# Kernel tuning notes

Hardware: AMD Instinct MI355X
Metric: run time of the kernel (lower is better)

Reference implementation:

```python
import jax, jax.numpy as jnp
import numpy as np

D_K = 64
SCALE = 1.0 / np.sqrt(D_K).astype(np.float32)


def setup_inputs() -> dict:
    key = jax.random.key(0)
    kq, kk, kv = jax.random.split(key, 3)
    B, S, D = 4, 2048, 512
    q = jax.random.normal(kq, (B, S, D), dtype=jnp.float32)
    k = jax.random.normal(kk, (B, S, D), dtype=jnp.float32)
    v = jax.random.normal(kv, (B, S, D), dtype=jnp.float32)
    return {"q": q, "k": k, "v": v}


def reference(q, k, v):
    # n_head == 1: the per-head strided slices are the full tensors.
    # Original computes BOTH 'new_k' (scaled q@k^T) and 'new_v' (unscaled q@k^T);
    # note: v is never used in the original forward math (faithful reproduction).
    qk = jnp.einsum('bsd,btd->bst', q, k)           # [B, S, S]
    scores = qk * SCALE                              # new_k
    attn = jax.nn.softmax(scores, axis=2)            # softmax over dim 2
    # dropout with p=0.1 is identity in eval / deterministic reference
    out = jnp.matmul(attn, qk)                       # attn @ new_v -> [B, S, S]
    return out
```

## Files before the change

kernel.cpp:

```cpp
#include <hip/hip_runtime.h>
#include <hip/hip_bf16.h>
#include <stdint.h>


#define SS 2048
#define DD 512
#define BATCH 4
#define NTB 8
#define NT2A 32

typedef __attribute__((ext_vector_type(8))) short short8;
typedef __attribute__((ext_vector_type(8))) _Float16 half8;
typedef __attribute__((ext_vector_type(4))) float floatx4;
typedef __attribute__((ext_vector_type(4))) float float4v;
typedef __attribute__((ext_vector_type(4))) unsigned int uintx4;

#define GLOBAL_AS const __attribute__((address_space(1)))
#define LDS_AS __attribute__((address_space(3)))

__device__ __forceinline__ uint32_t pk2h(float x, float y) {
    _Float16 hx = (_Float16)x, hy = (_Float16)y;
    union { _Float16 h; uint16_t u; } cx, cy;
    cx.h = hx; cy.h = hy;
    return (uint32_t)cx.u | ((uint32_t)cy.u << 16);
}
__device__ __forceinline__ float h2f(uint32_t ubits) {
    union { uint16_t u; _Float16 h; } c; c.u = (uint16_t)ubits; return (float)c.h;
}
__device__ __forceinline__ uint16_t f2h(float f) {
    union { _Float16 h; uint16_t u; } c; c.h = (_Float16)f; return c.u;
}

union PackU { uint32_t u[4]; short8 s8; };

__global__ __launch_bounds__(256) void prep_kernel(
    const float* __restrict__ Q, const float* __restrict__ K,
    uint16_t* __restrict__ qT, uint16_t* __restrict__ qH,
    uint16_t* __restrict__ kH)
{
    const int b   = blockIdx.z;
    const int tid = threadIdx.x;

    if (blockIdx.y >= 8) {
        const float* src = (blockIdx.y == 8) ? (K + (size_t)b * SS * DD)
                                             : (Q + (size_t)b * SS * DD);
        uint16_t* dst = (blockIdx.y == 8) ? (kH + (size_t)b * SS * DD)
                                          : (qH + (size_t)b * SS * DD);
        const int g0 = blockIdx.x * 256 + tid;
#pragma unroll
        for (int i = 0; i < 16; ++i) {
            const int g = g0 + i * 8192;
            const float4v* s4 = (const float4v*)(src + (size_t)g * 8);
            float4v x0 = s4[0], x1 = s4[1];
            PackU p;
            p.u[0] = pk2h(x0[0], x0[1]);
            p.u[1] = pk2h(x0[2], x0[3]);
            p.u[2] = pk2h(x1[0], x1[1]);
            p.u[3] = pk2h(x1[2], x1[3]);
            *(short8*)(dst + (size_t)g * 8) = p.s8;
        }
        return;
    }

    const int u0 = blockIdx.x * 64;
    const int d0 = blockIdx.y * 64;
    const float* qb = Q + (size_t)b * SS * DD;
    uint16_t* qTb = qT + (size_t)b * DD * SS;

    __shared__ uint16_t T[64 * 66];

    {
        const int r  = tid >> 2;
        const int c4 = (tid & 3) * 16;
        const float* src = qb + (size_t)(u0 + r) * DD + d0 + c4;
        float4v x0 = *(const float4v*)(src + 0);
        float4v x1 = *(const float4v*)(src + 4);
        float4v x2 = *(const float4v*)(src + 8);
        float4v x3 = *(const float4v*)(src + 12);
        uint32_t* tw = (uint32_t*)&T[r * 66 + c4];
        tw[0] = pk2h(x0[0], x0[1]); tw[1] = pk2h(x0[2], x0[3]);
        tw[2] = pk2h(x1[0], x1[1]); tw[3] = pk2h(x1[2], x1[3]);
        tw[4] = pk2h(x2[0], x2[1]); tw[5] = pk2h(x2[2], x2[3]);
        tw[6] = pk2h(x3[0], x3[1]); tw[7] = pk2h(x3[2], x3[3]);
    }
    __syncthreads();
#pragma unroll
    for (int p = 0; p < 2; ++p) {
        const int dl  = (tid >> 3) + p * 32;
        const int ul8 = (tid & 7) * 8;
        uint16_t t8[8];
#pragma unroll
        for (int j = 0; j < 8; ++j) t8[j] = T[(ul8 + j) * 66 + dl];
        PackU o;
        o.u[0] = (uint32_t)t8[0] | ((uint32_t)t8[1] << 16);
        o.u[1] = (uint32_t)t8[2] | ((uint32_t)t8[3] << 16);
        o.u[2] = (uint32_t)t8[4] | ((uint32_t)t8[5] << 16);
        o.u[3] = (uint32_t)t8[6] | ((uint32_t)t8[7] << 16);
        *(short8*)(&qTb[(size_t)(d0 + dl) * SS + u0 + ul8]) = o.s8;
    }
}

__global__ __launch_bounds__(512, 2) void gemm1_kernel(
    const uint16_t* __restrict__ qH, const uint16_t* __restrict__ kH,
    uint16_t* __restrict__ qk)
{
    const int b  = blockIdx.z;
    const int s0 = blockIdx.y * 256;
    const int t0 = blockIdx.x * 256;
    const uint16_t* ab = qH + (size_t)b * SS * DD;
    const uint16_t* bb = kH + (size_t)b * SS * DD;

    __shared__ uint16_t smem[65536];

    const int tid  = threadIdx.x;
    const int lane = tid & 63;
    const int wave = tid >> 6;
    const int wm   = wave >> 2;
    const int wn   = wave & 3;
    const int fm   = lane & 15;
    const int quad = lane >> 4;

    floatx4 acc[8][4];
#pragma unroll
    for (int i = 0; i < 8; ++i)
#pragma unroll
        for (int j = 0; j < 4; ++j)
            acc[i][j] = (floatx4)0.0f;

    const int sl0  = (quad ^ (fm & 7)) * 8;
    const int aoff = (wm * 128 + fm) * 64;
    const int boff = 32768 + (wn * 64 + fm) * 64;

    const int c0 = wave * 128 + lane;
    const int r0 = c0 >> 3;  const int l0 = ((c0 & 7) ^ (r0 & 7)) * 8;
    const int c1 = c0 + 64;
    const int r1 = c1 >> 3;  const int l1 = ((c1 & 7) ^ (r1 & 7)) * 8;
    const int ldsW = wave * 1024;

    auto STAGE_A = [&](int tt, int h) {
        uint16_t* base = &smem[(tt & 1) * 16384 + h * 8192 + ldsW];
        __builtin_amdgcn_global_load_lds(
            (GLOBAL_AS void*)(ab + (size_t)(s0 + h * 128 + r0) * DD + tt * 64 + l0),
            (LDS_AS void*)(base), 16, 0, 0);
        __builtin_amdgcn_global_load_lds(
            (GLOBAL_AS void*)(ab + (size_t)(s0 + h * 128 + r1) * DD + tt * 64 + l1),
            (LDS_AS void*)(base + 512), 16, 0, 0);
    };
    auto STAGE_B = [&](int tt, int h) {
        uint16_t* base = &smem[32768 + (tt & 1) * 16384 + h * 8192 + ldsW];
        __builtin_amdgcn_global_load_lds(
            (GLOBAL_AS void*)(bb + (size_t)(t0 + h * 128 + r0) * DD + tt * 64 + l0),
            (LDS_AS void*)(base), 16, 0, 0);
        __builtin_amdgcn_global_load_lds(
            (GLOBAL_AS void*)(bb + (size_t)(t0 + h * 128 + r1) * DD + tt * 64 + l1),
            (LDS_AS void*)(base + 512), 16, 0, 0);
    };

    STAGE_A(0, 0); STAGE_A(0, 1); STAGE_B(0, 0); STAGE_B(0, 1);
    STAGE_B(1, 0); STAGE_B(1, 1);
    asm volatile("s_waitcnt vmcnt(4)" ::: "memory");
    __builtin_amdgcn_s_barrier();

    half8 aF[4], aF2[4], bF[4][2];

    for (int t = 0; t < NTB; ++t) {
        const int abase = (t & 1) * 16384;
        const int bbase = (t & 1) * 16384;

#pragma unroll
        for (int nt = 0; nt < 4; ++nt) {
            bF[nt][0] = *(const half8*)&smem[bbase + boff + nt * 1024 + sl0];
            bF[nt][1] = *(const half8*)&smem[bbase + boff + nt * 1024 + (sl0 ^ 32)];
        }
#pragma unroll
        for (int m = 0; m < 4; ++m)
            aF[m] = *(const half8*)&smem[abase + aoff + m * 1024 + sl0];
        if (t + 1 < NTB) STAGE_A(t + 1, 0);
        __builtin_amdgcn_s_barrier();
        asm volatile("s_waitcnt lgkmcnt(0)" ::: "memory");
        __builtin_amdgcn_s_setprio(1);
#pragma unroll
        for (int m = 0; m < 4; ++m)
#pragma unroll
            for (int nt = 0; nt < 4; ++nt)
                acc[m][nt] = __builtin_amdgcn_mfma_f32_16x16x32_f16(aF[m], bF[nt][0], acc[m][nt], 0, 0, 0);
        __builtin_amdgcn_s_setprio(0);
        __builtin_amdgcn_s_barrier();

#pragma unroll
        for (int m = 0; m < 4; ++m)
            aF2[m] = *(const half8*)&smem[abase + aoff + (m + 4) * 1024 + sl0];
        if (t + 1 < NTB) STAGE_A(t + 1, 1);
        __builtin_amdgcn_s_barrier();
        asm volatile("s_waitcnt lgkmcnt(0)" ::: "memory");
        __builtin_amdgcn_s_setprio(1);
#pragma unroll
        for (int m = 0; m < 4; ++m)
#pragma unroll
            for (int nt = 0; nt < 4; ++nt)
                acc[m + 4][nt] = __builtin_amdgcn_mfma_f32_16x16x32_f16(aF2[m], bF[nt][0], acc[m + 4][nt], 0, 0, 0);
        __builtin_amdgcn_s_setprio(0);
        __builtin_amdgcn_s_barrier();

#pragma unroll
        for (int m = 0; m < 4; ++m)
            aF[m] = *(const half8*)&smem[abase + aoff + m * 1024 + (sl0 ^ 32)];
        if (t + 2 < NTB) STAGE_B(t + 2, 0);
        __builtin_amdgcn_s_barrier();
        asm volatile("s_waitcnt lgkmcnt(0)" ::: "memory");
        __builtin_amdgcn_s_setprio(1);
#pragma unroll
        for (int m = 0; m < 4; ++m)
#pragma unroll
            for (int nt = 0; nt < 4; ++nt)
                acc[m][nt] = __builtin_amdgcn_mfma_f32_16x16x32_f16(aF[m], bF[nt][1], acc[m][nt], 0, 0, 0);
        __builtin_amdgcn_s_setprio(0);
        __builtin_amdgcn_s_barrier();

#pragma unroll
        for (int m = 0; m < 4; ++m)
            aF2[m] = *(const half8*)&smem[abase + aoff + (m + 4) * 1024 + (sl0 ^ 32)];
        if (t + 2 < NTB) {
            STAGE_B(t + 2, 1);
            asm volatile("s_waitcnt vmcnt(4)" ::: "memory");
        } else {
            asm volatile("s_waitcnt vmcnt(0)" ::: "memory");
        }
        __builtin_amdgcn_s_barrier();
        asm volatile("s_waitcnt lgkmcnt(0)" ::: "memory");
        __builtin_amdgcn_s_setprio(1);
#pragma unroll
        for (int m = 0; m < 4; ++m)
#pragma unroll
            for (int nt = 0; nt < 4; ++nt)
                acc[m + 4][nt] = __builtin_amdgcn_mfma_f32_16x16x32_f16(aF2[m], bF[nt][1], acc[m + 4][nt], 0, 0, 0);
        __builtin_amdgcn_s_setprio(0);
        __builtin_amdgcn_s_barrier();
    }

    uint16_t* ob = qk + (size_t)b * SS * SS;
#pragma unroll
    for (int mt = 0; mt < 8; ++mt) {
#pragma unroll
        for (int nt = 0; nt < 4; ++nt) {
            const int srow = s0 + wm * 128 + mt * 16 + quad * 4;
            const int tcol = t0 + wn * 64 + nt * 16 + fm;
#pragma unroll
            for (int reg = 0; reg < 4; ++reg)
                ob[(size_t)(srow + reg) * SS + tcol] = f2h(acc[mt][nt][reg]);
        }
    }
}

__global__ __launch_bounds__(256) void softmax_inplace(uint16_t* __restrict__ qk)
{
    const size_t row = blockIdx.x;
    uint16_t* x = qk + row * SS;
    const int tid  = threadIdx.x;
    const int lane = tid & 63;
    const int wave = tid >> 6;

    uintx4 raw = *(const uintx4*)(x + tid * 8);
    float v[8];
#pragma unroll
    for (int i = 0; i < 4; ++i) {
        uint32_t u = raw[i];
        v[2 * i]     = h2f(u & 0xffffu) * 0.125f;
        v[2 * i + 1] = h2f(u >> 16) * 0.125f;
    }
    float m = v[0];
#pragma unroll
    for (int j = 1; j < 8; ++j) m = fmaxf(m, v[j]);
#pragma unroll
    for (int off = 1; off < 64; off <<= 1) m = fmaxf(m, __shfl_xor(m, off, 64));
    __shared__ float red[8];
    if (lane == 0) red[wave] = m;
    __syncthreads();
    m = fmaxf(fmaxf(red[0], red[1]), fmaxf(red[2], red[3]));

    float s = 0.f;
#pragma unroll
    for (int j = 0; j < 8; ++j) { v[j] = __expf(v[j] - m); s += v[j]; }
#pragma unroll
    for (int off = 1; off < 64; off <<= 1) s += __shfl_xor(s, off, 64);
    if (lane == 0) red[4 + wave] = s;
    __syncthreads();
    s = (red[4] + red[5]) + (red[6] + red[7]);
    const float inv = 1.0f / s;
#pragma unroll
    for (int i = 0; i < 4; ++i)
        raw[i] = pk2h(v[2 * i] * inv, v[2 * i + 1] * inv);
    *(uintx4*)(x + tid * 8) = raw;
}

__global__ __launch_bounds__(512, 2) void gemm2a_kernel(
    const uint16_t* __restrict__ attn, const uint16_t* __restrict__ qT,
    uint16_t* __restrict__ tmp)
{
    const int b  = blockIdx.z;
    const int s0 = blockIdx.y * 128;
    const int t0 = blockIdx.x * 128;
    const uint16_t* ab = attn + (size_t)b * SS * SS;
    const uint16_t* bb = qT   + (size_t)b * DD * SS;

    __shared__ uint16_t smem[32768];

    const int tid  = threadIdx.x;
    const int lane = tid & 63;
    const int wave = tid >> 6;
    const int wm   = wave >> 2;
    const int wn   = wave & 3;
    const int fm   = lane & 15;
    const int quad = lane >> 4;

    floatx4 acc[4][2];
#pragma unroll
    for (int i = 0; i < 4; ++i)
#pragma unroll
        for (int j = 0; j < 2; ++j)
            acc[i][j] = (floatx4)0.0f;

    const int sl0  = (quad ^ (fm & 7)) * 8;
    const int aoff = (wm * 64 + fm) * 64;
    const int boff = 16384 + (wn * 32 + fm) * 64;

    const int r0 = tid >> 3;
    const int l0 = (((tid & 7) ^ (r0 & 7))) * 8;
    const int r1 = r0 + 64;
    const int l1 = (((tid & 7) ^ (r1 & 7))) * 8;
    const int ldsW = wave * 512;

    auto STAGE_A = [&](int tt) {
        uint16_t* base = &smem[(tt & 1) * 8192 + ldsW];
        __builtin_amdgcn_global_load_lds(
            (GLOBAL_AS void*)(ab + (size_t)(s0 + r0) * SS + tt * 64 + l0),
            (LDS_AS void*)(base), 16, 0, 0);
        __builtin_amdgcn_global_load_lds(
            (GLOBAL_AS void*)(ab + (size_t)(s0 + r1) * SS + tt * 64 + l1),
            (LDS_AS void*)(base + 4096), 16, 0, 0);
    };
    auto STAGE_B = [&](int tt) {
        uint16_t* base = &smem[16384 + (tt & 1) * 8192 + ldsW];
        __builtin_amdgcn_global_load_lds(
            (GLOBAL_AS void*)(bb + (size_t)(t0 + r0) * SS + tt * 64 + l0),
            (LDS_AS void*)(base), 16, 0, 0);
        __builtin_amdgcn_global_load_lds(
            (GLOBAL_AS void*)(bb + (size_t)(t0 + r1) * SS + tt * 64 + l1),
            (LDS_AS void*)(base + 4096), 16, 0, 0);
    };

    STAGE_A(0); STAGE_B(0); STAGE_A(1); STAGE_B(1);
    asm volatile("s_waitcnt vmcnt(4)" ::: "memory");
    __builtin_amdgcn_s_barrier();

    half8 aF[4][2], bF[2][2];

    for (int t = 0; t < NT2A; ++t) {
        const int buf = (t & 1) * 8192;

#pragma unroll
        for (int m = 0; m < 4; ++m) {
            aF[m][0] = *(const half8*)&smem[buf + aoff + m * 1024 + sl0];
            aF[m][1] = *(const half8*)&smem[buf + aoff + m * 1024 + (sl0 ^ 32)];
        }
#pragma unroll
        for (int n = 0; n < 2; ++n) {
            bF[n][0] = *(const half8*)&smem[buf + boff + n * 1024 + sl0];
            bF[n][1] = *(const half8*)&smem[buf + boff + n * 1024 + (sl0 ^ 32)];
        }
        asm volatile("s_waitcnt lgkmcnt(0)" ::: "memory");
        __builtin_amdgcn_s_setprio(1);
#pragma unroll
        for (int m = 0; m < 4; ++m)
#pragma unroll
            for (int n = 0; n < 2; ++n)
                acc[m][n] = __builtin_amdgcn_mfma_f32_16x16x32_f16(aF[m][0], bF[n][0], acc[m][n], 0, 0, 0);
        __builtin_amdgcn_s_setprio(0);
        __builtin_amdgcn_s_barrier();

        if (t + 2 < NT2A) {
            STAGE_A(t + 2); STAGE_B(t + 2);
            asm volatile("s_waitcnt vmcnt(4)" ::: "memory");
        } else {
            asm volatile("s_waitcnt vmcnt(0)" ::: "memory");
        }
        __builtin_amdgcn_s_barrier();
        __builtin_amdgcn_s_setprio(1);
#pragma unroll
        for (int m = 0; m < 4; ++m)
#pragma unroll
            for (int n = 0; n < 2; ++n)
                acc[m][n] = __builtin_amdgcn_mfma_f32_16x16x32_f16(aF[m][1], bF[n][1], acc[m][n], 0, 0, 0);
        __builtin_amdgcn_s_setprio(0);
    }

    uint16_t* tb = tmp + (size_t)b * SS * DD;
#pragma unroll
    for (int mt = 0; mt < 4; ++mt) {
#pragma unroll
        for (int n = 0; n < 2; ++n) {
            const int srw  = s0 + wm * 64 + mt * 16 + quad * 4;
            const int tcol = t0 + wn * 32 + n * 16 + fm;
#pragma unroll
            for (int reg = 0; reg < 4; ++reg)
                tb[(size_t)(srw + reg) * DD + tcol] = f2h(acc[mt][n][reg]);
        }
    }
}

__global__ __launch_bounds__(512, 2) void gemm2b_kernel(
    const uint16_t* __restrict__ tmp, const uint16_t* __restrict__ kH,
    float* __restrict__ out)
{
    const int b  = blockIdx.z;
    const int s0 = blockIdx.y * 256;
    const int t0 = blockIdx.x * 256;
    const uint16_t* ab = tmp + (size_t)b * SS * DD;
    const uint16_t* bb = kH  + (size_t)b * SS * DD;

    __shared__ uint16_t smem[65536];

    const int tid  = threadIdx.x;
    const int lane = tid & 63;
    const int wave = tid >> 6;
    const int wm   = wave >> 2;
    const int wn   = wave & 3;
    const int fm   = lane & 15;
    const int quad = lane >> 4;

    floatx4 acc[8][4];
#pragma unroll
    for (int i = 0; i < 8; ++i)
#pragma unroll
        for (int j = 0; j < 4; ++j)
            acc[i][j] = (floatx4)0.0f;

    const int sl0  = (quad ^ (fm & 7)) * 8;
    const int aoff = (wm * 128 + fm) * 64;
    const int boff = 32768 + (wn * 64 + fm) * 64;

    const int c0 = wave * 128 + lane;
    const int r0 = c0 >> 3;  const int l0 = ((c0 & 7) ^ (r0 & 7)) * 8;
    const int c1 = c0 + 64;
    const int r1 = c1 >> 3;  const int l1 = ((c1 & 7) ^ (r1 & 7)) * 8;
    const int ldsW = wave * 1024;

    auto STAGE_A = [&](int tt, int h) {
        uint16_t* base = &smem[(tt & 1) * 16384 + h * 8192 + ldsW];
        __builtin_amdgcn_global_load_lds(
            (GLOBAL_AS void*)(ab + (size_t)(s0 + h * 128 + r0) * DD + tt * 64 + l0),
            (LDS_AS void*)(base), 16, 0, 0);
        __builtin_amdgcn_global_load_lds(
            (GLOBAL_AS void*)(ab + (size_t)(s0 + h * 128 + r1) * DD + tt * 64 + l1),
            (LDS_AS void*)(base + 512), 16, 0, 0);
    };
    auto STAGE_B = [&](int tt, int h) {
        uint16_t* base = &smem[32768 + (tt & 1) * 16384 + h * 8192 + ldsW];
        __builtin_amdgcn_global_load_lds(
            (GLOBAL_AS void*)(bb + (size_t)(t0 + h * 128 + r0) * DD + tt * 64 + l0),
            (LDS_AS void*)(base), 16, 0, 0);
        __builtin_amdgcn_global_load_lds(
            (GLOBAL_AS void*)(bb + (size_t)(t0 + h * 128 + r1) * DD + tt * 64 + l1),
            (LDS_AS void*)(base + 512), 16, 0, 0);
    };

    STAGE_A(0, 0); STAGE_A(0, 1); STAGE_B(0, 0); STAGE_B(0, 1);
    STAGE_B(1, 0); STAGE_B(1, 1);
    asm volatile("s_waitcnt vmcnt(4)" ::: "memory");
    __builtin_amdgcn_s_barrier();

    half8 aF[4], aF2[4], bF[4][2];

    for (int t = 0; t < NTB; ++t) {
        const int abase = (t & 1) * 16384;
        const int bbase = (t & 1) * 16384;

#pragma unroll
        for (int nt = 0; nt < 4; ++nt) {
            bF[nt][0] = *(const half8*)&smem[bbase + boff + nt * 1024 + sl0];
            bF[nt][1] = *(const half8*)&smem[bbase + boff + nt * 1024 + (sl0 ^ 32)];
        }
#pragma unroll
        for (int m = 0; m < 4; ++m)
            aF[m] = *(const half8*)&smem[abase + aoff + m * 1024 + sl0];
        if (t + 1 < NTB) STAGE_A(t + 1, 0);
        __builtin_amdgcn_s_barrier();
        asm volatile("s_waitcnt lgkmcnt(0)" ::: "memory");
        __builtin_amdgcn_s_setprio(1);
#pragma unroll
        for (int m = 0; m < 4; ++m)
#pragma unroll
            for (int nt = 0; nt < 4; ++nt)
                acc[m][nt] = __builtin_amdgcn_mfma_f32_16x16x32_f16(aF[m], bF[nt][0], acc[m][nt], 0, 0, 0);
        __builtin_amdgcn_s_setprio(0);
        __builtin_amdgcn_s_barrier();

#pragma unroll
        for (int m = 0; m < 4; ++m)
            aF2[m] = *(const half8*)&smem[abase + aoff + (m + 4) * 1024 + sl0];
        if (t + 1 < NTB) STAGE_A(t + 1, 1);
        __builtin_amdgcn_s_barrier();
        asm volatile("s_waitcnt lgkmcnt(0)" ::: "memory");
        __builtin_amdgcn_s_setprio(1);
#pragma unroll
        for (int m = 0; m < 4; ++m)
#pragma unroll
            for (int nt = 0; nt < 4; ++nt)
                acc[m + 4][nt] = __builtin_amdgcn_mfma_f32_16x16x32_f16(aF2[m], bF[nt][0], acc[m + 4][nt], 0, 0, 0);
        __builtin_amdgcn_s_setprio(0);
        __builtin_amdgcn_s_barrier();

#pragma unroll
        for (int m = 0; m < 4; ++m)
            aF[m] = *(const half8*)&smem[abase + aoff + m * 1024 + (sl0 ^ 32)];
        if (t + 2 < NTB) STAGE_B(t + 2, 0);
        __builtin_amdgcn_s_barrier();
        asm volatile("s_waitcnt lgkmcnt(0)" ::: "memory");
        __builtin_amdgcn_s_setprio(1);
#pragma unroll
        for (int m = 0; m < 4; ++m)
#pragma unroll
            for (int nt = 0; nt < 4; ++nt)
                acc[m][nt] = __builtin_amdgcn_mfma_f32_16x16x32_f16(aF[m], bF[nt][1], acc[m][nt], 0, 0, 0);
        __builtin_amdgcn_s_setprio(0);
        __builtin_amdgcn_s_barrier();

#pragma unroll
        for (int m = 0; m < 4; ++m)
            aF2[m] = *(const half8*)&smem[abase + aoff + (m + 4) * 1024 + (sl0 ^ 32)];
        if (t + 2 < NTB) {
            STAGE_B(t + 2, 1);
            asm volatile("s_waitcnt vmcnt(4)" ::: "memory");
        } else {
            asm volatile("s_waitcnt vmcnt(0)" ::: "memory");
        }
        __builtin_amdgcn_s_barrier();
        asm volatile("s_waitcnt lgkmcnt(0)" ::: "memory");
        __builtin_amdgcn_s_setprio(1);
#pragma unroll
        for (int m = 0; m < 4; ++m)
#pragma unroll
            for (int nt = 0; nt < 4; ++nt)
                acc[m + 4][nt] = __builtin_amdgcn_mfma_f32_16x16x32_f16(aF2[m], bF[nt][1], acc[m + 4][nt], 0, 0, 0);
        __builtin_amdgcn_s_setprio(0);
        __builtin_amdgcn_s_barrier();
    }

    float* ob = out + (size_t)b * SS * SS;
#pragma unroll
    for (int mt = 0; mt < 8; ++mt) {
#pragma unroll
        for (int nt = 0; nt < 4; ++nt) {
            const int srow = s0 + wm * 128 + mt * 16 + quad * 4;
            const int tcol = t0 + wn * 64 + nt * 16 + fm;
#pragma unroll
            for (int reg = 0; reg < 4; ++reg)
                ob[(size_t)(srow + reg) * SS + tcol] = acc[mt][nt][reg];
        }
    }
}

extern "C" void kernel_launch(void* const* d_in, const int* in_sizes, int n_in,
                              void* d_out, int out_size, void* d_ws, size_t ws_size,
                              hipStream_t stream) {
    const float* q = (const float*)d_in[0];
    const float* k = (const float*)d_in[1];
    float* out = (float*)d_out;

    uint16_t* qk  = (uint16_t*)d_ws;
    uint16_t* qT  = qk + (size_t)BATCH * SS * SS;
    uint16_t* qH  = qT + (size_t)BATCH * DD * SS;
    uint16_t* kH  = qH + (size_t)BATCH * SS * DD;
    uint16_t* tmp = kH + (size_t)BATCH * SS * DD;

    prep_kernel<<<dim3(32, 10, BATCH), 256, 0, stream>>>(q, k, qT, qH, kH);
    gemm1_kernel<<<dim3(SS / 256, SS / 256, BATCH), 512, 0, stream>>>(qH, kH, qk);
    softmax_inplace<<<dim3(BATCH * SS), 256, 0, stream>>>(qk);
    gemm2a_kernel<<<dim3(DD / 128, SS / 128, BATCH), 512, 0, stream>>>(qk, qT, tmp);
    gemm2b_kernel<<<dim3(SS / 256, SS / 256, BATCH), 512, 0, stream>>>(tmp, kH, out);
}
```

Baseline: 186.7 us.

## Fuse softmax normalization into gemm2a A-loading and merge Q fp16 conversion into transpose

The softmax kernel no longer writes normalized probabilities back. It only computes per-row max and inverse sum. gemm2a loads raw fp16 scores into registers, applies exp/scale/normalize, and writes the result to LDS instead of using direct global-to-LDS loads. This removes one full read-write pass over the B×S×S fp16 matrix. Separately, the prep kernel writes the fp16 Q copy from its transpose blocks, dropping the extra Q-conversion block row. In exchange, gemm2a recomputes exp for each column tile block (4x redundancy) and loses the async LDS load path for A.

```diff
diff --git a/kernel.cpp b/kernel.cpp
--- a/kernel.cpp
+++ b/kernel.cpp
@@ -41,11 +41,9 @@
     const int b   = blockIdx.z;
     const int tid = threadIdx.x;
 
-    if (blockIdx.y >= 8) {
-        const float* src = (blockIdx.y == 8) ? (K + (size_t)b * SS * DD)
-                                             : (Q + (size_t)b * SS * DD);
-        uint16_t* dst = (blockIdx.y == 8) ? (kH + (size_t)b * SS * DD)
-                                          : (qH + (size_t)b * SS * DD);
+    if (blockIdx.y == 8) {
+        const float* src = K + (size_t)b * SS * DD;
+        uint16_t* dst = kH + (size_t)b * SS * DD;
         const int g0 = blockIdx.x * 256 + tid;
 #pragma unroll
         for (int i = 0; i < 16; ++i) {
@@ -66,6 +64,7 @@
     const int d0 = blockIdx.y * 64;
     const float* qb = Q + (size_t)b * SS * DD;
     uint16_t* qTb = qT + (size_t)b * DD * SS;
+    uint16_t* qHb = qH + (size_t)b * SS * DD;
 
     __shared__ uint16_t T[64 * 66];
 
@@ -77,11 +76,18 @@
         float4v x1 = *(const float4v*)(src + 4);
         float4v x2 = *(const float4v*)(src + 8);
         float4v x3 = *(const float4v*)(src + 12);
+        uint32_t w0 = pk2h(x0[0], x0[1]), w1 = pk2h(x0[2], x0[3]);
+        uint32_t w2 = pk2h(x1[0], x1[1]), w3 = pk2h(x1[2], x1[3]);
+        uint32_t w4 = pk2h(x2[0], x2[1]), w5 = pk2h(x2[2], x2[3]);
+        uint32_t w6 = pk2h(x3[0], x3[1]), w7 = pk2h(x3[2], x3[3]);
         uint32_t* tw = (uint32_t*)&T[r * 66 + c4];
-        tw[0] = pk2h(x0[0], x0[1]); tw[1] = pk2h(x0[2], x0[3]);
-        tw[2] = pk2h(x1[0], x1[1]); tw[3] = pk2h(x1[2], x1[3]);
-        tw[4] = pk2h(x2[0], x2[1]); tw[5] = pk2h(x2[2], x2[3]);
-        tw[6] = pk2h(x3[0], x3[1]); tw[7] = pk2h(x3[2], x3[3]);
+        tw[0] = w0; tw[1] = w1; tw[2] = w2; tw[3] = w3;
+        tw[4] = w4; tw[5] = w5; tw[6] = w6; tw[7] = w7;
+        PackU p;
+        p.u[0] = w0; p.u[1] = w1; p.u[2] = w2; p.u[3] = w3;
+        *(short8*)(&qHb[(size_t)(u0 + r) * DD + d0 + c4]) = p.s8;
+        p.u[0] = w4; p.u[1] = w5; p.u[2] = w6; p.u[3] = w7;
+        *(short8*)(&qHb[(size_t)(u0 + r) * DD + d0 + c4 + 8]) = p.s8;
     }
     __syncthreads();
 #pragma unroll
@@ -252,10 +258,11 @@
     }
 }
 
-__global__ __launch_bounds__(256) void softmax_inplace(uint16_t* __restrict__ qk)
+__global__ __launch_bounds__(256) void rowstats_kernel(
+    const uint16_t* __restrict__ qk, float2* __restrict__ stats)
 {
     const size_t row = blockIdx.x;
-    uint16_t* x = qk + row * SS;
+    const uint16_t* x = qk + row * SS;
     const int tid  = threadIdx.x;
     const int lane = tid & 63;
     const int wave = tid >> 6;
@@ -280,28 +287,24 @@
 
     float s = 0.f;
 #pragma unroll
-    for (int j = 0; j < 8; ++j) { v[j] = __expf(v[j] - m); s += v[j]; }
+    for (int j = 0; j < 8; ++j) s += __expf(v[j] - m);
 #pragma unroll
     for (int off = 1; off < 64; off <<= 1) s += __shfl_xor(s, off, 64);
     if (lane == 0) red[4 + wave] = s;
     __syncthreads();
     s = (red[4] + red[5]) + (red[6] + red[7]);
-    const float inv = 1.0f / s;
-#pragma unroll
-    for (int i = 0; i < 4; ++i)
-        raw[i] = pk2h(v[2 * i] * inv, v[2 * i + 1] * inv);
-    *(uintx4*)(x + tid * 8) = raw;
+    if (tid == 0) stats[row] = make_float2(m, 1.0f / s);
 }
 
 __global__ __launch_bounds__(512, 2) void gemm2a_kernel(
-    const uint16_t* __restrict__ attn, const uint16_t* __restrict__ qT,
-    uint16_t* __restrict__ tmp)
+    const uint16_t* __restrict__ qk, const uint16_t* __restrict__ qT,
+    const float2* __restrict__ stats, uint16_t* __restrict__ tmp)
 {
     const int b  = blockIdx.z;
     const int s0 = blockIdx.y * 128;
     const int t0 = blockIdx.x * 128;
-    const uint16_t* ab = attn + (size_t)b * SS * SS;
-    const uint16_t* bb = qT   + (size_t)b * DD * SS;
+    const uint16_t* ab = qk + (size_t)b * SS * SS;
+    const uint16_t* bb = qT + (size_t)b * DD * SS;
 
     __shared__ uint16_t smem[32768];
 
@@ -327,17 +330,35 @@
     const int r0 = tid >> 3;
     const int l0 = (((tid & 7) ^ (r0 & 7))) * 8;
     const int r1 = r0 + 64;
-    const int l1 = (((tid & 7) ^ (r1 & 7))) * 8;
+    const int l1 = l0;
     const int ldsW = wave * 512;
 
-    auto STAGE_A = [&](int tt) {
-        uint16_t* base = &smem[(tt & 1) * 8192 + ldsW];
-        __builtin_amdgcn_global_load_lds(
-            (GLOBAL_AS void*)(ab + (size_t)(s0 + r0) * SS + tt * 64 + l0),
-            (LDS_AS void*)(base), 16, 0, 0);
-        __builtin_amdgcn_global_load_lds(
-            (GLOBAL_AS void*)(ab + (size_t)(s0 + r1) * SS + tt * 64 + l1),
-            (LDS_AS void*)(base + 4096), 16, 0, 0);
+    const float2 st0 = stats[(size_t)b * SS + s0 + r0];
+    const float2 st1 = stats[(size_t)b * SS + s0 + r1];
+
+    auto LOAD_A = [&](int tt, uintx4& ua, uintx4& ub) {
+        ua = *(const uintx4*)(ab + (size_t)(s0 + r0) * SS + tt * 64 + l0);
+        ub = *(const uintx4*)(ab + (size_t)(s0 + r1) * SS + tt * 64 + l1);
+    };
+    auto WRITE_A = [&](int tt, const uintx4& ua, const uintx4& ub) {
+        uint16_t* base = &smem[(tt & 1) * 8192 + ldsW + lane * 8];
+        PackU p;
+#pragma unroll
+        for (int j = 0; j < 4; ++j) {
+            uint32_t u = ua[j];
+            float va = h2f(u & 0xffffu) * 0.125f;
+            float vb = h2f(u >> 16) * 0.125f;
+            p.u[j] = pk2h(__expf(va - st0.x) * st0.y, __expf(vb - st0.x) * st0.y);
+        }
+        *(short8*)base = p.s8;
+#pragma unroll
+        for (int j = 0; j < 4; ++j) {
+            uint32_t u = ub[j];
+            float va = h2f(u & 0xffffu) * 0.125f;
+            float vb = h2f(u >> 16) * 0.125f;
+            p.u[j] = pk2h(__expf(va - st1.x) * st1.y, __expf(vb - st1.x) * st1.y);
+        }
+        *(short8*)(base + 4096) = p.s8;
     };
     auto STAGE_B = [&](int tt) {
         uint16_t* base = &smem[16384 + (tt & 1) * 8192 + ldsW];
@@ -349,8 +370,15 @@
             (LDS_AS void*)(base + 4096), 16, 0, 0);
     };
 
-    STAGE_A(0); STAGE_B(0); STAGE_A(1); STAGE_B(1);
-    asm volatile("s_waitcnt vmcnt(4)" ::: "memory");
+    uintx4 a0a, a0b, a1a, a1b;
+    LOAD_A(0, a0a, a0b);
+    LOAD_A(1, a1a, a1b);
+    asm volatile("" ::: "memory");
+    STAGE_B(0); STAGE_B(1);
+    asm volatile("s_waitcnt vmcnt(2)" ::: "memory");
+    WRITE_A(0, a0a, a0b);
+    WRITE_A(1, a1a, a1b);
+    asm volatile("s_waitcnt lgkmcnt(0)" ::: "memory");
     __builtin_amdgcn_s_barrier();
 
     half8 aF[4][2], bF[2][2];
@@ -358,6 +386,7 @@
     for (int t = 0; t < NT2A; ++t) {
         const int buf = (t & 1) * 8192;
 
+        uintx4 nA0, nA1;
 #pragma unroll
         for (int m = 0; m < 4; ++m) {
             aF[m][0] = *(const half8*)&smem[buf + aoff + m * 1024 + sl0];
@@ -368,6 +397,7 @@
             bF[n][0] = *(const half8*)&smem[buf + boff + n * 1024 + sl0];
             bF[n][1] = *(const half8*)&smem[buf + boff + n * 1024 + (sl0 ^ 32)];
         }
+        if (t + 2 < NT2A) LOAD_A(t + 2, nA0, nA1);
         asm volatile("s_waitcnt lgkmcnt(0)" ::: "memory");
         __builtin_amdgcn_s_setprio(1);
 #pragma unroll
@@ -379,8 +409,10 @@
         __builtin_amdgcn_s_barrier();
 
         if (t + 2 < NT2A) {
-            STAGE_A(t + 2); STAGE_B(t + 2);
-            asm volatile("s_waitcnt vmcnt(4)" ::: "memory");
+            STAGE_B(t + 2);
+            asm volatile("s_waitcnt vmcnt(2)" ::: "memory");
+            WRITE_A(t + 2, nA0, nA1);
+            asm volatile("s_waitcnt lgkmcnt(0)" ::: "memory");
         } else {
             asm volatile("s_waitcnt vmcnt(0)" ::: "memory");
         }
@@ -572,10 +604,11 @@
     uint16_t* qH  = qT + (size_t)BATCH * DD * SS;
     uint16_t* kH  = qH + (size_t)BATCH * SS * DD;
     uint16_t* tmp = kH + (size_t)BATCH * SS * DD;
-
-    prep_kernel<<<dim3(32, 10, BATCH), 256, 0, stream>>>(q, k, qT, qH, kH);
+    float2* stats = (float2*)(tmp + (size_t)BATCH * SS * DD);
+
+    prep_kernel<<<dim3(32, 9, BATCH), 256, 0, stream>>>(q, k, qT, qH, kH);
     gemm1_kernel<<<dim3(SS / 256, SS / 256, BATCH), 512, 0, stream>>>(qH, kH, qk);
-    softmax_inplace<<<dim3(BATCH * SS), 256, 0, stream>>>(qk);
-    gemm2a_kernel<<<dim3(DD / 128, SS / 128, BATCH), 512, 0, stream>>>(qk, qT, tmp);
+    rowstats_kernel<<<dim3(BATCH * SS), 256, 0, stream>>>(qk, stats);
+    gemm2a_kernel<<<dim3(DD / 128, SS / 128, BATCH), 512, 0, stream>>>(qk, qT, stats, tmp);
     gemm2b_kernel<<<dim3(SS / 256, SS / 256, BATCH), 512, 0, stream>>>(tmp, kH, out);
 }
```

After: 204.4 us. 9.5% more time.
